# Kernel tuning notes

Hardware: AMD Instinct MI355X
Metric: run time of the kernel (lower is better)

The kernel has to match this reference:

```python
import jax, jax.numpy as jnp
from jax import lax
import numpy as np

NUM_STEPS = 20
GATE_TIME = 1.0
DT = GATE_TIME / NUM_STEPS
BATCH = 8388608  # number of qubit states (columns)


def setup_inputs() -> dict:
    key = jax.random.key(0)
    k1, k2 = jax.random.split(key)
    # learnable pulse amplitudes, initialized to 2.0 as in the torch module
    amplitudes = jnp.full((NUM_STEPS,), 2.0, dtype=jnp.float32)
    state_real = jax.random.normal(k1, (2, BATCH), dtype=jnp.float32)
    state_imag = jax.random.normal(k2, (2, BATCH), dtype=jnp.float32)
    return {"amplitudes": amplitudes, "state_real": state_real, "state_imag": state_imag}


def reference(amplitudes, state_real, state_imag):
    # H_k = (a_k / 2) * X ;  U_k = exp(-i * H_k * dt) = cos(a_k*dt/2) I - i sin(a_k*dt/2) X
    # (exact closed form of matrix_exp for the Pauli-X generator)
    state = state_real + 1j * state_imag  # [2, B] complex64

    def step(s, a):
        theta = a * (DT * 0.5)
        c = jnp.cos(theta)
        sn = jnp.sin(theta)
        # X @ s swaps the two rows
        s_new = c * s - 1j * sn * s[::-1, :]
        return s_new, None

    state, _ = lax.scan(step, state, amplitudes)
    # return real-valued view [2(real/imag), 2, B]
    return jnp.stack([state.real, state.imag])
```

## Files before the change

### kernel.cpp

```cpp
#include <hip/hip_runtime.h>


#define BLOCK 256
#define UNROLL 4

typedef float v4f __attribute__((ext_vector_type(4)));

__global__ __launch_bounds__(BLOCK) void grape_kernel(
    const float* __restrict__ amps, int nsteps,
    const v4f* __restrict__ sreal, const v4f* __restrict__ simag,
    v4f* __restrict__ out, long long B4) {
    float theta = 0.0f;
    for (int k = 0; k < nsteps; ++k) theta += amps[k];
    theta *= 0.5f / (float)nsteps;
    const float c = cosf(theta);
    const float s = sinf(theta);

    const long long nth = (long long)gridDim.x * BLOCK;
    const long long tid = (long long)blockIdx.x * BLOCK + threadIdx.x;

    const v4f* __restrict__ r0p = sreal;
    const v4f* __restrict__ r1p = sreal + B4;
    const v4f* __restrict__ i0p = simag;
    const v4f* __restrict__ i1p = simag + B4;
    v4f* o0 = out;
    v4f* o1 = out + B4;
    v4f* o2 = out + 2 * B4;
    v4f* o3 = out + 3 * B4;

    v4f r0[UNROLL], r1[UNROLL], i0[UNROLL], i1[UNROLL];
#pragma unroll
    for (int u = 0; u < UNROLL; ++u) {
        long long j = tid + (long long)u * nth;
        long long jj = (j < B4) ? j : tid;
        r0[u] = r0p[jj];
        r1[u] = r1p[jj];
        i0[u] = i0p[jj];
        i1[u] = i1p[jj];
    }

#pragma unroll
    for (int u = 0; u < UNROLL; ++u) {
        long long j = tid + (long long)u * nth;
        if (j >= B4) break;
        v4f a = c * r0[u] + s * i1[u];
        v4f b = c * r1[u] + s * i0[u];
        v4f d = c * i0[u] - s * r1[u];
        v4f e = c * i1[u] - s * r0[u];
        __builtin_nontemporal_store(a, &o0[j]);
        __builtin_nontemporal_store(b, &o1[j]);
        __builtin_nontemporal_store(d, &o2[j]);
        __builtin_nontemporal_store(e, &o3[j]);
    }
}

extern "C" void kernel_launch(void* const* d_in, const int* in_sizes, int n_in,
                              void* d_out, int out_size, void* d_ws, size_t ws_size,
                              hipStream_t stream) {
    const float* amps  = (const float*)d_in[0];
    const float* sreal = (const float*)d_in[1];
    const float* simag = (const float*)d_in[2];
    float* out = (float*)d_out;

    int nsteps = in_sizes[0];
    long long B  = (long long)in_sizes[1] / 2;
    long long B4 = B / 4;

    long long per_block = (long long)BLOCK * UNROLL;
    long long grid = (B4 + per_block - 1) / per_block;

    grape_kernel<<<(dim3)(unsigned)grid, BLOCK, 0, stream>>>(
        amps, nsteps, (const v4f*)sreal, (const v4f*)simag,
        (v4f*)out, B4);
}
```

Before: 245.7 us.

## Split rotation into independent row pairs across blocks with two-vector per-thread work

Each block now handles only one of the two independent (real row, imag row) pairings of the X rotation, so each thread reads two input streams and writes two outputs instead of four each. Threads process two adjacent float4 vectors, and the grid is doubled to cover both pairings. This is meant to raise the number of concurrent blocks and reduce per-thread register pressure and address streams, at the cost of more blocks and bounds checks.

```diff
diff --git a/kernel.cpp b/kernel.cpp
--- a/kernel.cpp
+++ b/kernel.cpp
@@ -2,7 +2,6 @@
 
 
 #define BLOCK 256
-#define UNROLL 4
 
 typedef float v4f __attribute__((ext_vector_type(4)));
 
@@ -16,41 +15,44 @@
     const float c = cosf(theta);
     const float s = sinf(theta);
 
-    const long long nth = (long long)gridDim.x * BLOCK;
-    const long long tid = (long long)blockIdx.x * BLOCK + threadIdx.x;
+    const int pair = blockIdx.x & 1;
+    const long long pb = blockIdx.x >> 1;
+    const long long nb = gridDim.x >> 1;
 
-    const v4f* __restrict__ r0p = sreal;
-    const v4f* __restrict__ r1p = sreal + B4;
-    const v4f* __restrict__ i0p = simag;
-    const v4f* __restrict__ i1p = simag + B4;
-    v4f* o0 = out;
-    v4f* o1 = out + B4;
-    v4f* o2 = out + 2 * B4;
-    v4f* o3 = out + 3 * B4;
-
-    v4f r0[UNROLL], r1[UNROLL], i0[UNROLL], i1[UNROLL];
-#pragma unroll
-    for (int u = 0; u < UNROLL; ++u) {
-        long long j = tid + (long long)u * nth;
-        long long jj = (j < B4) ? j : tid;
-        r0[u] = r0p[jj];
-        r1[u] = r1p[jj];
-        i0[u] = i0p[jj];
-        i1[u] = i1p[jj];
+    const v4f* __restrict__ xin;
+    const v4f* __restrict__ yin;
+    v4f* oa;
+    v4f* ob;
+    if (pair == 0) {
+        xin = sreal;
+        yin = simag + B4;
+        oa  = out;
+        ob  = out + 3 * B4;
+    } else {
+        xin = sreal + B4;
+        yin = simag;
+        oa  = out + B4;
+        ob  = out + 2 * B4;
     }
 
-#pragma unroll
-    for (int u = 0; u < UNROLL; ++u) {
-        long long j = tid + (long long)u * nth;
-        if (j >= B4) break;
-        v4f a = c * r0[u] + s * i1[u];
-        v4f b = c * r1[u] + s * i0[u];
-        v4f d = c * i0[u] - s * r1[u];
-        v4f e = c * i1[u] - s * r0[u];
-        __builtin_nontemporal_store(a, &o0[j]);
-        __builtin_nontemporal_store(b, &o1[j]);
-        __builtin_nontemporal_store(d, &o2[j]);
-        __builtin_nontemporal_store(e, &o3[j]);
+    const long long stride = nb * (long long)BLOCK * 2;
+    for (long long j = (pb * BLOCK + threadIdx.x) * 2; j < B4; j += stride) {
+        v4f x0 = xin[j];
+        v4f x1 = (j + 1 < B4) ? xin[j + 1] : x0;
+        v4f y0 = yin[j];
+        v4f y1 = (j + 1 < B4) ? yin[j + 1] : y0;
+
+        v4f a0 = c * x0 + s * y0;
+        v4f a1 = c * x1 + s * y1;
+        v4f b0 = c * y0 - s * x0;
+        v4f b1 = c * y1 - s * x1;
+
+        __builtin_nontemporal_store(a0, &oa[j]);
+        __builtin_nontemporal_store(b0, &ob[j]);
+        if (j + 1 < B4) {
+            __builtin_nontemporal_store(a1, &oa[j + 1]);
+            __builtin_nontemporal_store(b1, &ob[j + 1]);
+        }
     }
 }
 
@@ -66,8 +68,8 @@
     long long B  = (long long)in_sizes[1] / 2;
     long long B4 = B / 4;
 
-    long long per_block = (long long)BLOCK * UNROLL;
-    long long grid = (B4 + per_block - 1) / per_block;
+    long long nb = (B4 + (long long)BLOCK * 2 - 1) / ((long long)BLOCK * 2);
+    long long grid = 2 * nb;
 
     grape_kernel<<<(dim3)(unsigned)grid, BLOCK, 0, stream>>>(
         amps, nsteps, (const v4f*)sreal, (const v4f*)simag,
```

After: 280.8 us. +14.3%, slower.
